# Kernel optimization log

Hardware: AMD Instinct MI355X
Metric: run time of the kernel (lower is better)

The kernel has to match this reference:

```python
import jax, jax.numpy as jnp
import numpy as np

D_MODEL = 1024
NUM_HEADS = 16
D_K = D_MODEL // NUM_HEADS
SCALE = 1.0 / np.sqrt(D_K).astype(np.float32)


def _rope_cos_sin(T, d_k):
    inv_freq = 1.0 / (10000.0 ** (jnp.arange(0, d_k, 2, dtype=jnp.float32) / d_k))
    t = jnp.arange(T, dtype=jnp.float32)
    freqs = jnp.outer(t, inv_freq)                      # [T, d_k/2]
    emb = jnp.concatenate([freqs, freqs], axis=-1)      # [T, d_k]
    return jnp.cos(emb)[None, None], jnp.sin(emb)[None, None]  # [1,1,T,d_k]


def _rotate_half(x):
    x1, x2 = x[..., : x.shape[-1] // 2], x[..., x.shape[-1] // 2 :]
    return jnp.concatenate([-x2, x1], axis=-1)


def setup_inputs() -> dict:
    key = jax.random.key(0)
    ks = jax.random.split(key, 8)
    B, T, C = 2, 2048, D_MODEL
    x = jax.random.normal(ks[0], (B, T, C), dtype=jnp.float32)
    # torch nn.Linear weights are [out, in]; forward does x @ W.T
    s = 1.0 / np.sqrt(C)
    Wq = jax.random.uniform(ks[1], (C, C), jnp.float32, -s, s)
    Wk = jax.random.uniform(ks[2], (C, C), jnp.float32, -s, s)
    Wv = jax.random.uniform(ks[3], (C, C), jnp.float32, -s, s)
    Wo = jax.random.uniform(ks[4], (C, C), jnp.float32, -s, s)
    bo = jax.random.uniform(ks[5], (C,), jnp.float32, -s, s)
    sector_bias = jnp.zeros((1, NUM_HEADS, 1, 1), dtype=jnp.float32)
    sector_weights = jax.random.uniform(ks[6], (B, T), jnp.float32, 0.5, 1.5)
    # causal mask, broadcastable to [B,H,T,T]; 0 -> masked
    mask = jnp.tril(jnp.ones((T, T), dtype=jnp.int32))[None, None]
    return {
        "x": x, "Wq": Wq, "Wk": Wk, "Wv": Wv, "Wo": Wo, "bo": bo,
        "sector_bias": sector_bias, "sector_weights": sector_weights,
        "mask": mask,
    }


def reference(x, Wq, Wk, Wv, Wo, bo, sector_bias, sector_weights, mask):
    B, T, C = x.shape
    H, dk = NUM_HEADS, D_K
    q = (x @ Wq.T).reshape(B, T, H, dk).transpose(0, 2, 1, 3)  # [B,H,T,dk]
    k = (x @ Wk.T).reshape(B, T, H, dk).transpose(0, 2, 1, 3)
    v = (x @ Wv.T).reshape(B, T, H, dk).transpose(0, 2, 1, 3)
    cos, sin = _rope_cos_sin(T, dk)
    q = q * cos + _rotate_half(q) * sin
    k = k * cos + _rotate_half(k) * sin
    scores = jnp.einsum("bhqd,bhkd->bhqk", q, k) * SCALE
    scores = scores + sector_bias
    scores = scores * sector_weights[:, None, None, :]  # broadcast over key dim
    scores = jnp.where(mask == 0, -jnp.inf, scores)
    attn = jax.nn.softmax(scores, axis=-1)
    out = jnp.einsum("bhqk,bhkd->bhqd", attn, v)
    out = out.transpose(0, 2, 1, 3).reshape(B, T, C)
    return out @ Wo.T + bo
```

## Files before the change

### kernel.cpp

```cpp
#include <hip/hip_runtime.h>


typedef __bf16 bf16x8 __attribute__((ext_vector_type(8)));
typedef float f32x4 __attribute__((ext_vector_type(4)));
typedef float f32x16 __attribute__((ext_vector_type(16)));
typedef unsigned short u16x8 __attribute__((ext_vector_type(8)));

__device__ __forceinline__ unsigned short f2bf(float f) {
    union { float f; unsigned int u; } c; c.f = f;
    unsigned int u = c.u;
    unsigned int r = u + 0x7fffu + ((u >> 16) & 1u);
    return (unsigned short)(r >> 16);
}
__device__ __forceinline__ void stage8_f32(unsigned short* dst, const float* src) {
    const float4 a = *(const float4*)src;
    const float4 b = *(const float4*)(src + 4);
    u16x8 v;
    v[0] = f2bf(a.x); v[1] = f2bf(a.y); v[2] = f2bf(a.z); v[3] = f2bf(a.w);
    v[4] = f2bf(b.x); v[5] = f2bf(b.y); v[6] = f2bf(b.z); v[7] = f2bf(b.w);
    *(u16x8*)dst = v;
}
__device__ __forceinline__ void async16(const unsigned short* g, unsigned short* l) {
    __builtin_amdgcn_global_load_lds(
        (const __attribute__((address_space(1))) void*)g,
        (__attribute__((address_space(3))) void*)l, 16, 0, 0);
}

__global__ __launch_bounds__(256) void cvt_all(
    const float* __restrict__ x, const float* __restrict__ Wq, const float* __restrict__ Wk,
    const float* __restrict__ Wv, const float* __restrict__ Wo,
    unsigned short* __restrict__ dst, int hasX, int n8)
{
    const int i = blockIdx.x * 256 + threadIdx.x;
    if (i >= n8) return;
    int r = i;
    const float* src; int off;
    const int xg = hasX ? 524288 : 0;
    if (r < xg) { src = x; off = r; }
    else {
        r -= xg;
        const int w = r >> 17, o = r & 131071;
        src = (w == 0) ? Wq : (w == 1) ? Wk : (w == 2) ? Wv : Wo;
        off = o;
    }
    stage8_f32(&dst[(size_t)i * 8], &src[(size_t)off * 8]);
}

template<int A_BF16>
__global__ __launch_bounds__(256) void gemm_qkv(
    const void* __restrict__ Av, const unsigned short* __restrict__ Wb,
    unsigned short* __restrict__ outv)
{
    constexpr int K = 1024, BK = 32;
    __shared__ __align__(16) unsigned short As[128 * BK];
    __shared__ __align__(16) unsigned short Bs[128 * BK];
    const int tid = threadIdx.x;
    const int wid = tid >> 6, lane = tid & 63, g = lane >> 4, l = lane & 15;
    const int wm = (wid & 1) * 64, wn = (wid >> 1) * 64;
    const int m0 = blockIdx.y * 128, n0 = blockIdx.x * 128;
    const int z = blockIdx.z;
    const unsigned short* W = Wb + (size_t)z * 1048576;

    f32x4 acc[4][4];
#pragma unroll
    for (int i = 0; i < 4; ++i)
#pragma unroll
        for (int j = 0; j < 4; ++j) acc[i][j] = f32x4{0.f, 0.f, 0.f, 0.f};

    const int r = tid >> 2;
    const int c = (tid & 3) * 8;
    unsigned short* AsW = &As[wid * 512];
    unsigned short* BsW = &Bs[wid * 512];

    for (int k0 = 0; k0 < K; k0 += BK) {
        __syncthreads();
        if (A_BF16) {
            const unsigned short* A = (const unsigned short*)Av;
            async16(&A[(size_t)(m0 + r) * K + k0 + c], AsW);
            async16(&A[(size_t)(m0 + 64 + r) * K + k0 + c], AsW + 2048);
        } else {
            const float* A = (const float*)Av;
            stage8_f32(&As[tid * 8],        &A[(size_t)(m0 + r) * K + k0 + c]);
            stage8_f32(&As[tid * 8 + 2048], &A[(size_t)(m0 + 64 + r) * K + k0 + c]);
        }
        async16(&W[(size_t)(n0 + r) * K + k0 + c], BsW);
        async16(&W[(size_t)(n0 + 64 + r) * K + k0 + c], BsW + 2048);
        __syncthreads();

        bf16x8 af[4], bfr[4];
#pragma unroll
        for (int im = 0; im < 4; ++im) af[im]  = *(const bf16x8*)&As[(wm + im * 16 + l) * BK + g * 8];
#pragma unroll
        for (int in = 0; in < 4; ++in) bfr[in] = *(const bf16x8*)&Bs[(wn + in * 16 + l) * BK + g * 8];
#pragma unroll
        for (int im = 0; im < 4; ++im)
#pragma unroll
            for (int in = 0; in < 4; ++in)
                acc[im][in] = __builtin_amdgcn_mfma_f32_16x16x32_bf16(af[im], bfr[in], acc[im][in], 0, 0, 0);
    }

    unsigned short* outq = outv + (size_t)z * 4194304;
    if (z < 2) {
        float freq[2];
#pragma unroll
        for (int in = 0; in < 2; ++in)
            freq[in] = exp2f(-(float)(in * 16 + l) * 0.41524101186f);
#pragma unroll
        for (int im = 0; im < 4; ++im)
#pragma unroll
            for (int i = 0; i < 4; ++i) {
                const int m = m0 + wm + im * 16 + g * 4 + i;
                const int b = m >> 11, t = m & 2047;
#pragma unroll
                for (int in = 0; in < 2; ++in) {
                    const int n = n0 + wn + in * 16 + l;
                    const int h = n >> 6, d = n & 63;
                    const float ang = (float)t * freq[in];
                    const float cs = __cosf(ang), sn = __sinf(ang);
                    const float x1 = acc[im][in][i], x2 = acc[im][in + 2][i];
                    const size_t bidx = (((size_t)b * 16 + h) * 2048 + t) << 6;
                    outq[bidx + d]      = f2bf(x1 * cs - x2 * sn);
                    outq[bidx + d + 32] = f2bf(x2 * cs + x1 * sn);
                }
            }
    } else {
#pragma unroll
        for (int im = 0; im < 4; ++im)
#pragma unroll
            for (int in = 0; in < 4; ++in) {
                const int n = n0 + wn + in * 16 + l;
                const int h = n >> 6, d = n & 63;
                const int mb = m0 + wm + im * 16 + g * 4;
                const int bq = mb >> 11, t0 = mb & 2047;
                ushort4 pk;
                pk.x = f2bf(acc[im][in][0]); pk.y = f2bf(acc[im][in][1]);
                pk.z = f2bf(acc[im][in][2]); pk.w = f2bf(acc[im][in][3]);
                *(ushort4*)&outq[((size_t)(bq * 16 + h)) * 131072 + (size_t)d * 2048 + t0] = pk;
            }
    }
}

__global__ __launch_bounds__(256) void gemm_proj(
    const unsigned short* __restrict__ A, const unsigned short* __restrict__ W,
    float* __restrict__ out, const float* __restrict__ bias)
{
    constexpr int K = 1024, BK = 32;
    __shared__ __align__(16) unsigned short As[64 * BK];
    __shared__ __align__(16) unsigned short Bs[128 * BK];
    const int tid = threadIdx.x;
    const int wid = tid >> 6, lane = tid & 63, g = lane >> 4, l = lane & 15;
    const int wm = (wid & 1) * 32, wn = (wid >> 1) * 64;
    const int m0 = blockIdx.y * 64, n0 = blockIdx.x * 128;

    f32x4 acc[2][4];
#pragma unroll
    for (int i = 0; i < 2; ++i)
#pragma unroll
        for (int j = 0; j < 4; ++j) acc[i][j] = f32x4{0.f, 0.f, 0.f, 0.f};

    const int r = tid >> 2;
    const int c = (tid & 3) * 8;
    unsigned short* AsW = &As[wid * 512];
    unsigned short* BsW = &Bs[wid * 512];

    for (int k0 = 0; k0 < K; k0 += BK) {
        __syncthreads();
        async16(&A[(size_t)(m0 + r) * K + k0 + c], AsW);
        async16(&W[(size_t)(n0 + r) * K + k0 + c], BsW);
        async16(&W[(size_t)(n0 + 64 + r) * K + k0 + c], BsW + 2048);
        __syncthreads();

        bf16x8 af[2], bfr[4];
#pragma unroll
        for (int im = 0; im < 2; ++im) af[im]  = *(const bf16x8*)&As[(wm + im * 16 + l) * BK + g * 8];
#pragma unroll
        for (int in = 0; in < 4; ++in) bfr[in] = *(const bf16x8*)&Bs[(wn + in * 16 + l) * BK + g * 8];
#pragma unroll
        for (int im = 0; im < 2; ++im)
#pragma unroll
            for (int in = 0; in < 4; ++in)
                acc[im][in] = __builtin_amdgcn_mfma_f32_16x16x32_bf16(af[im], bfr[in], acc[im][in], 0, 0, 0);
    }

#pragma unroll
    for (int im = 0; im < 2; ++im)
#pragma unroll
        for (int in = 0; in < 4; ++in) {
            const int n = n0 + wn + in * 16 + l;
#pragma unroll
            for (int i = 0; i < 4; ++i) {
                const int m = m0 + wm + im * 16 + g * 4 + i;
                out[(size_t)m * 1024 + n] = acc[im][in][i] + bias[n];
            }
        }
}

__global__ __launch_bounds__(128) void flash_attn(
    const unsigned short* __restrict__ Q, const unsigned short* __restrict__ Kg,
    const unsigned short* __restrict__ VT, const float* __restrict__ sbias,
    const float* __restrict__ sw, unsigned short* __restrict__ attn)
{
    constexpr int T = 2048;
    __shared__ __align__(16) unsigned short Mem[64 * 72 * 2 + 2 * 32 * 40];
    unsigned short* Ks  = Mem;
    unsigned short* VsT = Mem + 64 * 72;
    unsigned short* Ps  = Mem + 2 * 64 * 72;
    float* Cmb = (float*)Mem;

    const int tid = threadIdx.x, wid = tid >> 6, lane = tid & 63;
    const int hl = lane & 31, hh = lane >> 5;
    const int id = blockIdx.x;
    const int p  = 63 - (id >> 5);
    const int bh = id & 31, b = bh >> 4, h = bh & 15;
    const size_t base = (size_t)bh * T * 64;
    const size_t vtb  = (size_t)bh * 64 * T;
    const float bias = sbias[h];
    const float* swb = sw + b * T;

    bf16x8 onef;
#pragma unroll
    for (int j = 0; j < 8; ++j) onef[j] = (__bf16)1.0f;

    const int q0 = p * 32;
    bf16x8 qf[4];
#pragma unroll
    for (int ks = 0; ks < 4; ++ks)
        qf[ks] = *(const bf16x8*)&Q[base + (size_t)(q0 + hl) * 64 + ks * 16 + hh * 8];

    f32x16 oacc[2], lrow;
#pragma unroll
    for (int r = 0; r < 16; ++r) { oacc[0][r] = 0.f; oacc[1][r] = 0.f; lrow[r] = 0.f; }

    u16x8 kpre[4], vpre[4];
#pragma unroll
    for (int s = 0; s < 4; ++s) {
        const int ci = s * 128 + tid, rr = ci >> 3, c8 = (ci & 7) * 8;
        kpre[s] = *(const u16x8*)&Kg[base + (size_t)rr * 64 + c8];
        vpre[s] = *(const u16x8*)&VT[vtb + (size_t)rr * T + c8];
    }

    unsigned short* Pw = Ps + wid * 32 * 40;
    const int rounds = (p + 2) >> 1;
    for (int rd = 0; rd < rounds; ++rd) {
        const int k0 = rd * 64;
        __syncthreads();
#pragma unroll
        for (int s = 0; s < 4; ++s) {
            const int ci = s * 128 + tid, rr = ci >> 3, c8 = (ci & 7) * 8;
            *(u16x8*)&Ks[rr * 72 + c8]  = kpre[s];
            *(u16x8*)&VsT[rr * 72 + c8] = vpre[s];
        }
        __syncthreads();
        if (rd + 1 < rounds) {
            const int k1 = k0 + 64;
#pragma unroll
            for (int s = 0; s < 4; ++s) {
                const int ci = s * 128 + tid, rr = ci >> 3, c8 = (ci & 7) * 8;
                kpre[s] = *(const u16x8*)&Kg[base + (size_t)(k1 + rr) * 64 + c8];
                vpre[s] = *(const u16x8*)&VT[vtb + (size_t)rr * T + k1 + c8];
            }
        }

        const int kc = k0 + wid * 32 + hl;
        const float w = swb[kc];
        const float a = w * 0.125f, cst = w * bias;

        f32x16 sx;
#pragma unroll
        for (int r = 0; r < 16; ++r) sx[r] = 0.f;
#pragma unroll
        for (int ks = 0; ks < 4; ++ks) {
            const bf16x8 kf = *(const bf16x8*)&Ks[(wid * 32 + hl) * 72 + ks * 16 + hh * 8];
            sx = __builtin_amdgcn_mfma_f32_32x32x16_bf16(qf[ks], kf, sx, 0, 0, 0);
        }

#pragma unroll
        for (int r = 0; r < 16; ++r) {
            const int row = (r & 3) + 8 * (r >> 2) + 4 * hh;
            float xv = sx[r] * a + cst;
            xv = (kc <= q0 + row) ? xv : -1e30f;
            Pw[row * 40 + hl] = f2bf(__expf(xv));
        }
        __threadfence_block();
        bf16x8 pf[2];
        pf[0] = *(const bf16x8*)&Pw[hl * 40 + hh * 8];
        pf[1] = *(const bf16x8*)&Pw[hl * 40 + 16 + hh * 8];

        f32x16 ls;
#pragma unroll
        for (int r = 0; r < 16; ++r) ls[r] = 0.f;
        ls = __builtin_amdgcn_mfma_f32_32x32x16_bf16(pf[0], onef, ls, 0, 0, 0);
        ls = __builtin_amdgcn_mfma_f32_32x32x16_bf16(pf[1], onef, ls, 0, 0, 0);
#pragma unroll
        for (int r = 0; r < 16; ++r) lrow[r] += ls[r];

#pragma unroll
        for (int ks = 0; ks < 2; ++ks)
#pragma unroll
            for (int dt = 0; dt < 2; ++dt) {
                const bf16x8 vf = *(const bf16x8*)&VsT[(dt * 32 + hl) * 72 + wid * 32 + ks * 16 + hh * 8];
                oacc[dt] = __builtin_amdgcn_mfma_f32_32x32x16_bf16(pf[ks], vf, oacc[dt], 0, 0, 0);
            }
    }

    __syncthreads();
    if (wid == 1) {
#pragma unroll
        for (int dt = 0; dt < 2; ++dt)
#pragma unroll
            for (int r = 0; r < 16; ++r) Cmb[(dt * 16 + r) * 64 + lane] = oacc[dt][r];
#pragma unroll
        for (int r = 0; r < 16; ++r) Cmb[2048 + r * 64 + lane] = lrow[r];
    }
    __syncthreads();
    if (wid == 0) {
#pragma unroll
        for (int r = 0; r < 16; ++r) {
            const float li = 1.0f / (lrow[r] + Cmb[2048 + r * 64 + lane]);
            const int row = (r & 3) + 8 * (r >> 2) + 4 * hh;
            const int qr = q0 + row;
#pragma unroll
            for (int dt = 0; dt < 2; ++dt) {
                const float ov = oacc[dt][r] + Cmb[(dt * 16 + r) * 64 + lane];
                attn[(size_t)(b * T + qr) * 1024 + h * 64 + dt * 32 + hl] = f2bf(ov * li);
            }
        }
    }
}

extern "C" void kernel_launch(void* const* d_in, const int* in_sizes, int n_in,
                              void* d_out, int out_size, void* d_ws, size_t ws_size,
                              hipStream_t stream) {
    const float* x  = (const float*)d_in[0];
    const float* Wq = (const float*)d_in[1];
    const float* Wk = (const float*)d_in[2];
    const float* Wv = (const float*)d_in[3];
    const float* Wo = (const float*)d_in[4];
    const float* bo = (const float*)d_in[5];
    const float* sb = (const float*)d_in[6];
    const float* sw = (const float*)d_in[7];

    const size_t QKV_SZ = 4194304;
    const size_t W_SZ   = 1048576;
    unsigned short* ws16 = (unsigned short*)d_ws;
    const bool big = ws_size >= 2 * (4 * QKV_SZ + 4 * W_SZ);

    if (big) {
        unsigned short* xb    = ws16;
        unsigned short* Wb3   = xb + QKV_SZ;
        unsigned short* Wob   = Wb3 + 3 * W_SZ;
        unsigned short* qkv   = Wob + W_SZ;
        unsigned short* attnb = xb;

        cvt_all<<<4096, 256, 0, stream>>>(x, Wq, Wk, Wv, Wo, xb, 1, 1048576);
        gemm_qkv<1><<<dim3(8, 32, 3), 256, 0, stream>>>(xb, Wb3, qkv);
        flash_attn<<<2048, 128, 0, stream>>>(qkv, qkv + QKV_SZ, qkv + 2 * QKV_SZ,
                                             sb, sw, attnb);
        gemm_proj<<<dim3(8, 64), 256, 0, stream>>>(attnb, Wob, (float*)d_out, bo);
    } else {
        unsigned short* qkv   = ws16;
        unsigned short* attnb = qkv + 3 * QKV_SZ;
        unsigned short* Wb3   = attnb;
        unsigned short* Wob   = qkv;

        cvt_all<<<1536, 256, 0, stream>>>(x, Wq, Wk, Wv, Wo, Wb3, 0, 393216);
        gemm_qkv<0><<<dim3(8, 32, 3), 256, 0, stream>>>(x, Wb3, qkv);
        flash_attn<<<2048, 128, 0, stream>>>(qkv, qkv + QKV_SZ, qkv + 2 * QKV_SZ,
                                             sb, sw, attnb);
        cvt_all<<<512, 256, 0, stream>>>(x, Wo, Wo, Wo, Wo, Wob, 0, 131072);
        gemm_proj<<<dim3(8, 64), 256, 0, stream>>>(attnb, Wob, (float*)d_out, bo);
    }
}
```

Baseline: 225.4 us.

## Fold key weights into K, keep P in registers, skip masked tiles

The per-key sector weight, the softmax scale and log2(e) are now folded into K in the QKV GEMM epilogue, so the attention kernel works with exp2 and drops the per-element scaling. The probability tile no longer round-trips through LDS: it is packed with v_cvt_pk_bf16_f32 and rearranged across half-waves with permlane32_swap, with a shuffle fallback. Waves whose 32-key slice lies fully above the causal diagonal skip their MFMAs, and the row-sum accumulates straight into lrow. LDS shrinks and launch_bounds asks for 4 blocks, in exchange for bf16 rounding of the prescaled K and a bias path that is taken only when the bias is nonzero.

```diff
diff --git a/kernel.cpp b/kernel.cpp
--- a/kernel.cpp
+++ b/kernel.cpp
@@ -11,6 +11,23 @@
     unsigned int u = c.u;
     unsigned int r = u + 0x7fffu + ((u >> 16) & 1u);
     return (unsigned short)(r >> 16);
+}
+__device__ __forceinline__ unsigned cvtpk(float lo, float hi) {
+    unsigned r;
+    asm("v_cvt_pk_bf16_f32 %0, %1, %2" : "=v"(r) : "v"(lo), "v"(hi));
+    return r;
+}
+__device__ __forceinline__ void plswap(unsigned a, unsigned b, unsigned& r0, unsigned& r1) {
+#if __has_builtin(__builtin_amdgcn_permlane32_swap)
+    auto s = __builtin_amdgcn_permlane32_swap(a, b, false, false);
+    r0 = (unsigned)s[0]; r1 = (unsigned)s[1];
+#else
+    const int hh = (int)(threadIdx.x & 63) >> 5;
+    const unsigned oa = (unsigned)__shfl_xor((int)a, 32);
+    const unsigned ob = (unsigned)__shfl_xor((int)b, 32);
+    r0 = hh ? ob : a;
+    r1 = hh ? b : oa;
+#endif
 }
 __device__ __forceinline__ void stage8_f32(unsigned short* dst, const float* src) {
     const float4 a = *(const float4*)src;
@@ -49,7 +66,7 @@
 template<int A_BF16>
 __global__ __launch_bounds__(256) void gemm_qkv(
     const void* __restrict__ Av, const unsigned short* __restrict__ Wb,
-    unsigned short* __restrict__ outv)
+    unsigned short* __restrict__ outv, const float* __restrict__ swg)
 {
     constexpr int K = 1024, BK = 32;
     __shared__ __align__(16) unsigned short As[128 * BK];
@@ -111,6 +128,8 @@
             for (int i = 0; i < 4; ++i) {
                 const int m = m0 + wm + im * 16 + g * 4 + i;
                 const int b = m >> 11, t = m & 2047;
+                float fw = 1.0f;
+                if (z == 1) fw = 0.18033688011f * swg[(b << 11) + t];
 #pragma unroll
                 for (int in = 0; in < 2; ++in) {
                     const int n = n0 + wn + in * 16 + l;
@@ -119,8 +138,8 @@
                     const float cs = __cosf(ang), sn = __sinf(ang);
                     const float x1 = acc[im][in][i], x2 = acc[im][in + 2][i];
                     const size_t bidx = (((size_t)b * 16 + h) * 2048 + t) << 6;
-                    outq[bidx + d]      = f2bf(x1 * cs - x2 * sn);
-                    outq[bidx + d + 32] = f2bf(x2 * cs + x1 * sn);
+                    outq[bidx + d]      = f2bf((x1 * cs - x2 * sn) * fw);
+                    outq[bidx + d + 32] = f2bf((x2 * cs + x1 * sn) * fw);
                 }
             }
     } else {
@@ -195,16 +214,15 @@
         }
 }
 
-__global__ __launch_bounds__(128) void flash_attn(
+__global__ __launch_bounds__(128, 4) void flash_attn(
     const unsigned short* __restrict__ Q, const unsigned short* __restrict__ Kg,
     const unsigned short* __restrict__ VT, const float* __restrict__ sbias,
     const float* __restrict__ sw, unsigned short* __restrict__ attn)
 {
     constexpr int T = 2048;
-    __shared__ __align__(16) unsigned short Mem[64 * 72 * 2 + 2 * 32 * 40];
+    __shared__ __align__(16) unsigned short Mem[64 * 72 * 2];
     unsigned short* Ks  = Mem;
     unsigned short* VsT = Mem + 64 * 72;
-    unsigned short* Ps  = Mem + 2 * 64 * 72;
     float* Cmb = (float*)Mem;
 
     const int tid = threadIdx.x, wid = tid >> 6, lane = tid & 63;
@@ -239,7 +257,6 @@
         vpre[s] = *(const u16x8*)&VT[vtb + (size_t)rr * T + c8];
     }
 
-    unsigned short* Pw = Ps + wid * 32 * 40;
     const int rounds = (p + 2) >> 1;
     for (int rd = 0; rd < rounds; ++rd) {
         const int k0 = rd * 64;
@@ -261,46 +278,65 @@
             }
         }
 
-        const int kc = k0 + wid * 32 + hl;
-        const float w = swb[kc];
-        const float a = w * 0.125f, cst = w * bias;
-
-        f32x16 sx;
-#pragma unroll
-        for (int r = 0; r < 16; ++r) sx[r] = 0.f;
-#pragma unroll
-        for (int ks = 0; ks < 4; ++ks) {
-            const bf16x8 kf = *(const bf16x8*)&Ks[(wid * 32 + hl) * 72 + ks * 16 + hh * 8];
-            sx = __builtin_amdgcn_mfma_f32_32x32x16_bf16(qf[ks], kf, sx, 0, 0, 0);
-        }
-
-#pragma unroll
-        for (int r = 0; r < 16; ++r) {
-            const int row = (r & 3) + 8 * (r >> 2) + 4 * hh;
-            float xv = sx[r] * a + cst;
-            xv = (kc <= q0 + row) ? xv : -1e30f;
-            Pw[row * 40 + hl] = f2bf(__expf(xv));
-        }
-        __threadfence_block();
-        bf16x8 pf[2];
-        pf[0] = *(const bf16x8*)&Pw[hl * 40 + hh * 8];
-        pf[1] = *(const bf16x8*)&Pw[hl * 40 + 16 + hh * 8];
-
-        f32x16 ls;
-#pragma unroll
-        for (int r = 0; r < 16; ++r) ls[r] = 0.f;
-        ls = __builtin_amdgcn_mfma_f32_32x32x16_bf16(pf[0], onef, ls, 0, 0, 0);
-        ls = __builtin_amdgcn_mfma_f32_32x32x16_bf16(pf[1], onef, ls, 0, 0, 0);
-#pragma unroll
-        for (int r = 0; r < 16; ++r) lrow[r] += ls[r];
-
-#pragma unroll
-        for (int ks = 0; ks < 2; ++ks)
-#pragma unroll
-            for (int dt = 0; dt < 2; ++dt) {
-                const bf16x8 vf = *(const bf16x8*)&VsT[(dt * 32 + hl) * 72 + wid * 32 + ks * 16 + hh * 8];
-                oacc[dt] = __builtin_amdgcn_mfma_f32_32x32x16_bf16(pf[ks], vf, oacc[dt], 0, 0, 0);
-            }
+        const int kw0 = k0 + wid * 32;
+        if (kw0 <= q0 + 31) {
+            f32x16 sx;
+#pragma unroll
+            for (int r = 0; r < 16; ++r) sx[r] = 0.f;
+#pragma unroll
+            for (int ks = 0; ks < 4; ++ks) {
+                const bf16x8 kf = *(const bf16x8*)&Ks[(wid * 32 + hl) * 72 + ks * 16 + hh * 8];
+                sx = __builtin_amdgcn_mfma_f32_32x32x16_bf16(kf, qf[ks], sx, 0, 0, 0);
+            }
+            if (bias != 0.0f) {
+                const float bn = bias * 1.44269504f;
+#pragma unroll
+                for (int r = 0; r < 16; ++r) {
+                    const int kl = (r & 3) + 8 * (r >> 2) + 4 * hh;
+                    sx[r] += bn * swb[kw0 + kl];
+                }
+            }
+            if (kw0 + 31 > q0) {
+                const int dq = q0 + hl - kw0;
+#pragma unroll
+                for (int r = 0; r < 16; ++r) {
+                    const int kl = (r & 3) + 8 * (r >> 2) + 4 * hh;
+                    sx[r] = (kl <= dq) ? sx[r] : -1e30f;
+                }
+            }
+            float pr[16];
+#pragma unroll
+            for (int r = 0; r < 16; ++r) pr[r] = exp2f(sx[r]);
+
+            unsigned wds[8];
+#pragma unroll
+            for (int g2 = 0; g2 < 4; ++g2) {
+                wds[g2 * 2]     = cvtpk(pr[g2 * 4],     pr[g2 * 4 + 1]);
+                wds[g2 * 2 + 1] = cvtpk(pr[g2 * 4 + 2], pr[g2 * 4 + 3]);
+            }
+            bf16x8 pf[2];
+#pragma unroll
+            for (int ks = 0; ks < 2; ++ks) {
+                unsigned a0, a1, b0, b1;
+                plswap(wds[4 * ks],     wds[4 * ks + 2], a0, a1);
+                plswap(wds[4 * ks + 1], wds[4 * ks + 3], b0, b1);
+                union { unsigned u[4]; bf16x8 v; } pk_;
+                pk_.u[0] = a0; pk_.u[1] = b0;
+                pk_.u[2] = a1; pk_.u[3] = b1;
+                pf[ks] = pk_.v;
+            }
+
+            lrow = __builtin_amdgcn_mfma_f32_32x32x16_bf16(pf[0], onef, lrow, 0, 0, 0);
+            lrow = __builtin_amdgcn_mfma_f32_32x32x16_bf16(pf[1], onef, lrow, 0, 0, 0);
+
+#pragma unroll
+            for (int ks = 0; ks < 2; ++ks)
+#pragma unroll
+                for (int dt = 0; dt < 2; ++dt) {
+                    const bf16x8 vf = *(const bf16x8*)&VsT[(dt * 32 + hl) * 72 + wid * 32 + ks * 16 + hh * 8];
+                    oacc[dt] = __builtin_amdgcn_mfma_f32_32x32x16_bf16(pf[ks], vf, oacc[dt], 0, 0, 0);
+                }
+        }
     }
 
     __syncthreads();
@@ -353,7 +389,7 @@
         unsigned short* attnb = xb;
 
         cvt_all<<<4096, 256, 0, stream>>>(x, Wq, Wk, Wv, Wo, xb, 1, 1048576);
-        gemm_qkv<1><<<dim3(8, 32, 3), 256, 0, stream>>>(xb, Wb3, qkv);
+        gemm_qkv<1><<<dim3(8, 32, 3), 256, 0, stream>>>(xb, Wb3, qkv, sw);
         flash_attn<<<2048, 128, 0, stream>>>(qkv, qkv + QKV_SZ, qkv + 2 * QKV_SZ,
                                              sb, sw, attnb);
         gemm_proj<<<dim3(8, 64), 256, 0, stream>>>(attnb, Wob, (float*)d_out, bo);
@@ -364,7 +400,7 @@
         unsigned short* Wob   = qkv;
 
         cvt_all<<<1536, 256, 0, stream>>>(x, Wq, Wk, Wv, Wo, Wb3, 0, 393216);
-        gemm_qkv<0><<<dim3(8, 32, 3), 256, 0, stream>>>(x, Wb3, qkv);
+        gemm_qkv<0><<<dim3(8, 32, 3), 256, 0, stream>>>(x, Wb3, qkv, sw);
         flash_attn<<<2048, 128, 0, stream>>>(qkv, qkv + QKV_SZ, qkv + 2 * QKV_SZ,
                                              sb, sw, attnb);
         cvt_all<<<512, 256, 0, stream>>>(x, Wo, Wo, Wo, Wo, Wob, 0, 131072);
```

After: 322.7 us. 1.43x slower.
